# Optimization experiments

Measured on AMD Instinct MI355X. Metric: run time of the kernel, lower is better.

## Reference

```python
import jax, jax.numpy as jnp
import numpy as np
import math

HIDDEN_DIM = 1024
NUM_HEADS = 16
HEAD_DIM = HIDDEN_DIM // NUM_HEADS  # 64

def setup_inputs() -> dict:
    key = jax.random.key(0)
    k1, k2, k3 = jax.random.split(key, 3)
    x = jax.random.normal(k1, (8, 4096, HIDDEN_DIM), dtype=jnp.float32)
    W = jax.random.normal(k2, (HIDDEN_DIM, NUM_HEADS), dtype=jnp.float32) * (1.0 / math.sqrt(HIDDEN_DIM))
    mask = jax.random.randint(k3, (8, 4096), 0, 2, dtype=jnp.int32)
    return {"x": x, "W": W, "mask": mask}

def reference(x, W, mask):
    B, S, D = x.shape
    # linear scoring: [B,S,H], scaled by sqrt(head_dim)
    logits = jnp.einsum('bsd,dh->bsh', x, W) / math.sqrt(HEAD_DIM)
    # mask out padded positions (mask==0 -> -inf) before softmax over seq axis
    logits = jnp.where(mask[:, :, None] == 0, -jnp.inf, logits)
    attn = jax.nn.softmax(logits, axis=1)  # softmax over sequence dim
    # dropout is identity in eval mode
    # weighted sum: original expands x over heads, so each head pools the full hidden vector
    pooled = jnp.einsum('bsh,bsd->bhd', attn, x)  # [B, H, D]
    return pooled.reshape(B, NUM_HEADS * D)
```

## Files before the change

kernel.cpp:

```cpp
#include <hip/hip_runtime.h>
#include <math.h>

#define BB 8
#define SS 4096
#define DD 1024
#define HH 16

typedef __attribute__((ext_vector_type(4))) float f32x4;
typedef __fp16 fp16x2 __attribute__((ext_vector_type(2)));
typedef _Float16 half8v __attribute__((ext_vector_type(8)));


__device__ __forceinline__ void sm_merge(float& m, float& z, float om, float oz) {
  float nm = fmaxf(m, om);
  if (nm > -INFINITY)
    z = z * __expf(m - nm) + oz * __expf(om - nm);
  m = nm;
}

__global__ __launch_bounds__(256) void k_prepw(
    const float* __restrict__ W, ushort* __restrict__ wh16, ushort* __restrict__ wl16) {
  int i = blockIdx.x * 256 + threadIdx.x;
  int t = i >> 9;
  int l = (i >> 3) & 63;
  int e = i & 7;
  int d = t * 32 + (l >> 4) * 8 + e;
  int h = l & 15;
  float w = W[d * HH + h];
  _Float16 wh = (_Float16)w;
  _Float16 wl = (_Float16)(w - (float)wh);
  union { _Float16 f; ushort u; } ch, cl;
  ch.f = wh; cl.f = wl;
  wh16[i] = ch.u;
  wl16[i] = cl.u;
}

#define XLOAD(dst, c)                                                          \
  _Pragma("unroll") for (int k = 0; k < 8; ++k) {                              \
    int row = k * 2 + (lane >> 5);                                             \
    dst[k] = *reinterpret_cast<const float4*>(                                 \
        xw + (size_t)row * DD + (c) * 128 + (lane & 31) * 4);                  \
  }
#define XSTAGE(src, c)                                                         \
  _Pragma("unroll") for (int k = 0; k < 8; ++k) {                              \
    int row = k * 2 + (lane >> 5);                                             \
    lds4[(c) & 1][wv][row][(lane & 31) ^ (row & 7)] = src[k];                  \
  }
#define WLOAD(c)                                                               \
  _Pragma("unroll") for (int j = 0; j < 4; ++j) {                              \
    whf[(c) & 1][j] = bhp[(4 * (c) + j) * 64];                                 \
    wlf[(c) & 1][j] = blp[(4 * (c) + j) * 64];                                 \
  }

__global__ __launch_bounds__(256, 2) void k_logits(
    const float* __restrict__ x, const ushort* __restrict__ wh16,
    const ushort* __restrict__ wl16, const int* __restrict__ mask,
    float* __restrict__ plog, float2* __restrict__ bred) {
  __shared__ float4 lds4[2][4][16][32];
  __shared__ float2 smch[4][16];

  const int tid = threadIdx.x;
  const int lane = tid & 63;
  const int wv = __builtin_amdgcn_readfirstlane(tid >> 6);
  const int b = blockIdx.x >> 6;
  const int tile = blockIdx.x & 63;
  const int s0 = tile * 64;
  const int r15 = lane & 15;
  const int kg = lane >> 4;

  const float* xw = x + ((size_t)b * SS + s0 + wv * 16) * DD;
  const half8v* bhp = reinterpret_cast<const half8v*>(wh16) + lane;
  const half8v* blp = reinterpret_cast<const half8v*>(wl16) + lane;

  f32x4 acch = {0.f, 0.f, 0.f, 0.f};
  f32x4 accl = {0.f, 0.f, 0.f, 0.f};
  float4 st[2][8];
  half8v whf[2][4], wlf[2][4];

  XLOAD(st[0], 0);
  XLOAD(st[1], 1);
  XSTAGE(st[0], 0);
  WLOAD(0);
  WLOAD(1);

#pragma unroll
  for (int c = 0; c < 8; ++c) {
    if (c < 6) { XLOAD(st[c & 1], c + 2); }

#pragma unroll
    for (int t4 = 0; t4 < 4; ++t4) {
      const int u0 = t4 * 8 + kg * 2;
      float4 va = lds4[c & 1][wv][r15][u0 ^ (r15 & 7)];
      float4 vb = lds4[c & 1][wv][r15][(u0 + 1) ^ (r15 & 7)];
      union { fp16x2 h2[4]; half8v h8; } ax;
      ax.h2[0] = __builtin_amdgcn_cvt_pkrtz(va.x, va.y);
      ax.h2[1] = __builtin_amdgcn_cvt_pkrtz(va.z, va.w);
      ax.h2[2] = __builtin_amdgcn_cvt_pkrtz(vb.x, vb.y);
      ax.h2[3] = __builtin_amdgcn_cvt_pkrtz(vb.z, vb.w);
      acch = __builtin_amdgcn_mfma_f32_16x16x32_f16(ax.h8, whf[c & 1][t4], acch, 0, 0, 0);
      accl = __builtin_amdgcn_mfma_f32_16x16x32_f16(ax.h8, wlf[c & 1][t4], accl, 0, 0, 0);
    }

    if (c < 6) { WLOAD(c + 2); }
    if (c < 7) { XSTAGE(st[(c + 1) & 1], c + 1); }
  }

  float lv[4];
  float* ob = plog + ((size_t)b * SS + s0 + wv * 16) * HH;
#pragma unroll
  for (int q = 0; q < 4; ++q) {
    int srw = kg * 4 + q;
    int msk = mask[b * SS + s0 + wv * 16 + srw];
    float v = (acch[q] + accl[q]) * 0.125f;
    lv[q] = msk ? v : -INFINITY;
    ob[(size_t)srw * HH + r15] = lv[q];
  }
  float ml = fmaxf(fmaxf(lv[0], lv[1]), fmaxf(lv[2], lv[3]));
  float zl = 0.f;
  if (ml > -INFINITY) {
#pragma unroll
    for (int q = 0; q < 4; ++q) zl += __expf(lv[q] - ml);
  }
#pragma unroll
  for (int off = 16; off < 64; off <<= 1) {
    float om = __shfl_xor(ml, off, 64);
    float oz = __shfl_xor(zl, off, 64);
    sm_merge(ml, zl, om, oz);
  }
  if (kg == 0) smch[wv][r15] = make_float2(ml, zl);
  __syncthreads();
  if (tid < 16) {
    float2 p0 = smch[0][tid];
    float m = p0.x, z = p0.y;
#pragma unroll
    for (int w = 1; w < 4; ++w) {
      float2 pw = smch[w][tid];
      sm_merge(m, z, pw.x, pw.y);
    }
    bred[((size_t)b * 64 + tile) * HH + tid] = make_float2(m, z);
  }
}

__global__ __launch_bounds__(256) void k_pool(
    const float* __restrict__ x, const float* __restrict__ plog,
    const float2* __restrict__ bred, const int* __restrict__ mask,
    float* __restrict__ partial) {
  __shared__ float wl[128][16];
  __shared__ float fm[16], fz[16];
  const int tid = threadIdx.x;
  const int dh = blockIdx.x & 1;
  const int sc = (blockIdx.x >> 1) & 31;
  const int b = blockIdx.x >> 6;
  const int s0 = sc * 128;

  if (tid < 16) {
    float m = -INFINITY, z = 0.f;
#pragma unroll 4
    for (int c = 0; c < 64; ++c) {
      float2 p = bred[((size_t)b * 64 + c) * HH + tid];
      sm_merge(m, z, p.x, p.y);
    }
    fm[tid] = m;
    fz[tid] = (z > 0.f) ? 1.0f / z : 0.f;
  }
  __syncthreads();

  const float4* p0 = reinterpret_cast<const float4*>(plog + ((size_t)b * SS + s0) * HH);
  const int* mb = mask + b * SS + s0;
#pragma unroll
  for (int k = 0; k < 2; ++k) {
    int f = k * 256 + tid;
    float4 va = p0[f];
    int msk = mb[f >> 2];
    int hb = (f & 3) * 4;
    float4 w;
    w.x = msk ? __expf(va.x - fm[hb + 0]) * fz[hb + 0] : 0.f;
    w.y = msk ? __expf(va.y - fm[hb + 1]) * fz[hb + 1] : 0.f;
    w.z = msk ? __expf(va.z - fm[hb + 2]) * fz[hb + 2] : 0.f;
    w.w = msk ? __expf(va.w - fm[hb + 3]) * fz[hb + 3] : 0.f;
    *reinterpret_cast<float4*>(&wl[0][0] + f * 4) = w;
  }
  __syncthreads();

  float2 acc[HH];
#pragma unroll
  for (int h = 0; h < HH; ++h) acc[h] = make_float2(0.f, 0.f);

  const float* xb = x + ((size_t)b * SS + s0) * DD + dh * 512 + tid * 2;
  for (int s = 0; s < 128; ++s) {
    float2 xv = *reinterpret_cast<const float2*>(xb + (size_t)s * DD);
    const float4* wrow = reinterpret_cast<const float4*>(wl[s]);
    float4 wa = wrow[0], wb_ = wrow[1], wc = wrow[2], wd = wrow[3];
    float wvv[16] = {wa.x, wa.y, wa.z, wa.w, wb_.x, wb_.y, wb_.z, wb_.w,
                     wc.x, wc.y, wc.z, wc.w, wd.x, wd.y, wd.z, wd.w};
#pragma unroll
    for (int h = 0; h < HH; ++h) {
      float w = wvv[h];
      acc[h].x += w * xv.x;
      acc[h].y += w * xv.y;
    }
  }

  float* pb = partial + ((size_t)sc * BB + b) * (HH * DD) + dh * 512 + tid * 2;
#pragma unroll
  for (int h = 0; h < HH; ++h)
    *reinterpret_cast<float2*>(pb + (size_t)h * DD) = acc[h];
}

__global__ __launch_bounds__(256) void k_reduce(
    const float* __restrict__ partial, float* __restrict__ out) {
  const int idx = blockIdx.x * 256 + threadIdx.x;
  float s = 0.f;
#pragma unroll
  for (int c = 0; c < 32; ++c) s += partial[(size_t)c * (BB * HH * DD) + idx];
  out[idx] = s;
}

extern "C" void kernel_launch(void* const* d_in, const int* in_sizes, int n_in,
                              void* d_out, int out_size, void* d_ws, size_t ws_size,
                              hipStream_t stream) {
  const float* x = (const float*)d_in[0];
  const float* W = (const float*)d_in[1];
  const int* mask = (const int*)d_in[2];
  float* out = (float*)d_out;

  char* ws = (char*)d_ws;
  float* plog    = (float*)ws;
  float* partial = (float*)(ws + (size_t)6 * 1024 * 1024);
  ushort* wh16   = (ushort*)(ws + (size_t)22 * 1024 * 1024);
  ushort* wl16   = (ushort*)(ws + (size_t)22 * 1024 * 1024 + 32 * 1024);
  float2* bred   = (float2*)(ws + (size_t)23 * 1024 * 1024);

  k_prepw<<<64, 256, 0, stream>>>(W, wh16, wl16);
  k_logits<<<512, 256, 0, stream>>>(x, wh16, wl16, mask, plog, bred);
  k_pool<<<512, 256, 0, stream>>>(x, plog, bred, mask, partial);
  k_reduce<<<512, 256, 0, stream>>>(partial, out);
}
```

Before: 71.44 us.

## Split logits K-dimension across waves with 16-row tiles and more blocks

```diff
diff --git a/kernel.cpp b/kernel.cpp
--- a/kernel.cpp
+++ b/kernel.cpp
@@ -35,109 +35,91 @@
   wl16[i] = cl.u;
 }
 
-#define XLOAD(dst, c)                                                          \
-  _Pragma("unroll") for (int k = 0; k < 8; ++k) {                              \
-    int row = k * 2 + (lane >> 5);                                             \
-    dst[k] = *reinterpret_cast<const float4*>(                                 \
-        xw + (size_t)row * DD + (c) * 128 + (lane & 31) * 4);                  \
-  }
-#define XSTAGE(src, c)                                                         \
-  _Pragma("unroll") for (int k = 0; k < 8; ++k) {                              \
-    int row = k * 2 + (lane >> 5);                                             \
-    lds4[(c) & 1][wv][row][(lane & 31) ^ (row & 7)] = src[k];                  \
-  }
-#define WLOAD(c)                                                               \
-  _Pragma("unroll") for (int j = 0; j < 4; ++j) {                              \
-    whf[(c) & 1][j] = bhp[(4 * (c) + j) * 64];                                 \
-    wlf[(c) & 1][j] = blp[(4 * (c) + j) * 64];                                 \
-  }
-
 __global__ __launch_bounds__(256, 2) void k_logits(
     const float* __restrict__ x, const ushort* __restrict__ wh16,
     const ushort* __restrict__ wl16, const int* __restrict__ mask,
     float* __restrict__ plog, float2* __restrict__ bred) {
-  __shared__ float4 lds4[2][4][16][32];
-  __shared__ float2 smch[4][16];
+  __shared__ float4 xt[16][256];
+  __shared__ float red[4][16][16];
+  __shared__ float lt[16][17];
 
   const int tid = threadIdx.x;
   const int lane = tid & 63;
-  const int wv = __builtin_amdgcn_readfirstlane(tid >> 6);
-  const int b = blockIdx.x >> 6;
-  const int tile = blockIdx.x & 63;
-  const int s0 = tile * 64;
+  const int wv = tid >> 6;
+  const int b = blockIdx.x >> 8;
+  const int tile = blockIdx.x & 255;
   const int r15 = lane & 15;
   const int kg = lane >> 4;
 
-  const float* xw = x + ((size_t)b * SS + s0 + wv * 16) * DD;
+  const float* xbase = x + ((size_t)b * SS + tile * 16) * DD;
+
+  float4 stv[16];
+#pragma unroll
+  for (int rr = 0; rr < 4; ++rr) {
+#pragma unroll
+    for (int q = 0; q < 4; ++q)
+      stv[rr * 4 + q] = *reinterpret_cast<const float4*>(
+          xbase + (size_t)(wv * 4 + rr) * DD + q * 256 + lane * 4);
+  }
+#pragma unroll
+  for (int rr = 0; rr < 4; ++rr) {
+    int row = wv * 4 + rr;
+#pragma unroll
+    for (int q = 0; q < 4; ++q) {
+      int slot = q * 64 + lane;
+      xt[row][slot ^ (row & 7)] = stv[rr * 4 + q];
+    }
+  }
+  __syncthreads();
+
   const half8v* bhp = reinterpret_cast<const half8v*>(wh16) + lane;
   const half8v* blp = reinterpret_cast<const half8v*>(wl16) + lane;
 
   f32x4 acch = {0.f, 0.f, 0.f, 0.f};
   f32x4 accl = {0.f, 0.f, 0.f, 0.f};
-  float4 st[2][8];
-  half8v whf[2][4], wlf[2][4];
-
-  XLOAD(st[0], 0);
-  XLOAD(st[1], 1);
-  XSTAGE(st[0], 0);
-  WLOAD(0);
-  WLOAD(1);
-
-#pragma unroll
-  for (int c = 0; c < 8; ++c) {
-    if (c < 6) { XLOAD(st[c & 1], c + 2); }
-
-#pragma unroll
-    for (int t4 = 0; t4 < 4; ++t4) {
-      const int u0 = t4 * 8 + kg * 2;
-      float4 va = lds4[c & 1][wv][r15][u0 ^ (r15 & 7)];
-      float4 vb = lds4[c & 1][wv][r15][(u0 + 1) ^ (r15 & 7)];
-      union { fp16x2 h2[4]; half8v h8; } ax;
-      ax.h2[0] = __builtin_amdgcn_cvt_pkrtz(va.x, va.y);
-      ax.h2[1] = __builtin_amdgcn_cvt_pkrtz(va.z, va.w);
-      ax.h2[2] = __builtin_amdgcn_cvt_pkrtz(vb.x, vb.y);
-      ax.h2[3] = __builtin_amdgcn_cvt_pkrtz(vb.z, vb.w);
-      acch = __builtin_amdgcn_mfma_f32_16x16x32_f16(ax.h8, whf[c & 1][t4], acch, 0, 0, 0);
-      accl = __builtin_amdgcn_mfma_f32_16x16x32_f16(ax.h8, wlf[c & 1][t4], accl, 0, 0, 0);
-    }
-
-    if (c < 6) { WLOAD(c + 2); }
-    if (c < 7) { XSTAGE(st[(c + 1) & 1], c + 1); }
-  }
-
-  float lv[4];
-  float* ob = plog + ((size_t)b * SS + s0 + wv * 16) * HH;
-#pragma unroll
-  for (int q = 0; q < 4; ++q) {
-    int srw = kg * 4 + q;
-    int msk = mask[b * SS + s0 + wv * 16 + srw];
-    float v = (acch[q] + accl[q]) * 0.125f;
-    lv[q] = msk ? v : -INFINITY;
-    ob[(size_t)srw * HH + r15] = lv[q];
-  }
-  float ml = fmaxf(fmaxf(lv[0], lv[1]), fmaxf(lv[2], lv[3]));
-  float zl = 0.f;
-  if (ml > -INFINITY) {
-#pragma unroll
-    for (int q = 0; q < 4; ++q) zl += __expf(lv[q] - ml);
-  }
-#pragma unroll
-  for (int off = 16; off < 64; off <<= 1) {
-    float om = __shfl_xor(ml, off, 64);
-    float oz = __shfl_xor(zl, off, 64);
-    sm_merge(ml, zl, om, oz);
-  }
-  if (kg == 0) smch[wv][r15] = make_float2(ml, zl);
-  __syncthreads();
+#pragma unroll
+  for (int t = 0; t < 8; ++t) {
+    const int tg = wv * 8 + t;
+    half8v bh = bhp[tg * 64];
+    half8v bl = blp[tg * 64];
+    const int slot = wv * 64 + t * 8 + kg * 2;
+    float4 va = xt[r15][slot ^ (r15 & 7)];
+    float4 vb = xt[r15][(slot + 1) ^ (r15 & 7)];
+    union { fp16x2 h2[4]; half8v h8; } ax;
+    ax.h2[0] = __builtin_amdgcn_cvt_pkrtz(va.x, va.y);
+    ax.h2[1] = __builtin_amdgcn_cvt_pkrtz(va.z, va.w);
+    ax.h2[2] = __builtin_amdgcn_cvt_pkrtz(vb.x, vb.y);
+    ax.h2[3] = __builtin_amdgcn_cvt_pkrtz(vb.z, vb.w);
+    acch = __builtin_amdgcn_mfma_f32_16x16x32_f16(ax.h8, bh, acch, 0, 0, 0);
+    accl = __builtin_amdgcn_mfma_f32_16x16x32_f16(ax.h8, bl, accl, 0, 0, 0);
+  }
+
+#pragma unroll
+  for (int q = 0; q < 4; ++q)
+    red[wv][kg * 4 + q][r15] = acch[q] + accl[q];
+  __syncthreads();
+
+  {
+    const int s = tid >> 4, h = tid & 15;
+    float v = (red[0][s][h] + red[1][s][h] + red[2][s][h] + red[3][s][h]) * 0.125f;
+    int msk = mask[b * SS + tile * 16 + s];
+    float lv = msk ? v : -INFINITY;
+    plog[((size_t)b * SS + tile * 16 + s) * HH + h] = lv;
+    lt[s][h] = lv;
+  }
+  __syncthreads();
+
   if (tid < 16) {
-    float2 p0 = smch[0][tid];
-    float m = p0.x, z = p0.y;
-#pragma unroll
-    for (int w = 1; w < 4; ++w) {
-      float2 pw = smch[w][tid];
-      sm_merge(m, z, pw.x, pw.y);
-    }
-    bred[((size_t)b * 64 + tile) * HH + tid] = make_float2(m, z);
+    float m = -INFINITY;
+    for (int s = 0; s < 16; ++s) m = fmaxf(m, lt[s][tid]);
+    float Z = 0.f;
+    if (m > -INFINITY) {
+      for (int s = 0; s < 16; ++s) {
+        float v = lt[s][tid];
+        Z += (v > -INFINITY) ? __expf(v - m) : 0.f;
+      }
+    }
+    bred[((size_t)b * 256 + tile) * HH + tid] = make_float2(m, Z);
   }
 }
 
@@ -146,6 +128,7 @@
     const float2* __restrict__ bred, const int* __restrict__ mask,
     float* __restrict__ partial) {
   __shared__ float wl[128][16];
+  __shared__ float2 red2[16][16];
   __shared__ float fm[16], fz[16];
   const int tid = threadIdx.x;
   const int dh = blockIdx.x & 1;
@@ -153,11 +136,22 @@
   const int b = blockIdx.x >> 6;
   const int s0 = sc * 128;
 
+  {
+    const int h = tid & 15, cg = tid >> 4;
+    float m = -INFINITY, z = 0.f;
+#pragma unroll 4
+    for (int i = 0; i < 16; ++i) {
+      float2 p = bred[((size_t)b * 256 + cg * 16 + i) * HH + h];
+      sm_merge(m, z, p.x, p.y);
+    }
+    red2[cg][h] = make_float2(m, z);
+  }
+  __syncthreads();
   if (tid < 16) {
     float m = -INFINITY, z = 0.f;
-#pragma unroll 4
-    for (int c = 0; c < 64; ++c) {
-      float2 p = bred[((size_t)b * 64 + c) * HH + tid];
+#pragma unroll
+    for (int g = 0; g < 16; ++g) {
+      float2 p = red2[g][tid];
       sm_merge(m, z, p.x, p.y);
     }
     fm[tid] = m;
@@ -232,7 +226,7 @@
   float2* bred   = (float2*)(ws + (size_t)23 * 1024 * 1024);
 
   k_prepw<<<64, 256, 0, stream>>>(W, wh16, wl16);
-  k_logits<<<512, 256, 0, stream>>>(x, wh16, wl16, mask, plog, bred);
+  k_logits<<<2048, 256, 0, stream>>>(x, wh16, wl16, mask, plog, bred);
   k_pool<<<512, 256, 0, stream>>>(x, plog, bred, mask, partial);
   k_reduce<<<512, 256, 0, stream>>>(partial, out);
 }
```

Measured after the change: 72.03 us. Within noise of the previous version (+0.8%).
